# Performance work log

Hardware: AMD Instinct MI355X
Metric: run time of the kernel (lower is better)

## Reference

```python
import jax, jax.numpy as jnp
import numpy as np

DIM = 1024
BATCH = 16384
NUM_LAYERS = 6
S_E = 0.1   # strength_entail
S_C = 0.1   # strength_contra
S_N = 0.05  # strength_neutral
S_NB = 0.05 # strength_neutral_boost
EPS = 1e-12


def _normalize(x, axis=-1):
    # matches F.normalize: x / max(||x||, eps)
    n = jnp.sqrt(jnp.sum(x * x, axis=axis, keepdims=True))
    return x / jnp.maximum(n, EPS)


def setup_inputs() -> dict:
    key = jax.random.key(0)
    ks = jax.random.split(key, 8)
    return {
        "h0": jax.random.normal(ks[0], (BATCH, DIM), dtype=jnp.float32),
        "W1": jax.random.normal(ks[1], (DIM, DIM), dtype=jnp.float32) * 0.02,
        "b1": jnp.zeros((DIM,), dtype=jnp.float32),
        "W2": jax.random.normal(ks[2], (DIM, DIM), dtype=jnp.float32) * 0.02,
        "b2": jnp.zeros((DIM,), dtype=jnp.float32),
        "anchor_entail": jax.random.normal(ks[3], (DIM,), dtype=jnp.float32),
        "anchor_contra": jax.random.normal(ks[4], (DIM,), dtype=jnp.float32),
        "anchor_neutral": jax.random.normal(ks[5], (DIM,), dtype=jnp.float32),
    }


def reference(h0, W1, b1, W2, b2, anchor_entail, anchor_contra, anchor_neutral):
    # Static collapse with three fixed anchors (rot_rank=0, adaptive_metric=False).
    e_dir = _normalize(anchor_entail, axis=0)   # [D]
    c_dir = _normalize(anchor_contra, axis=0)
    n_dir = _normalize(anchor_neutral, axis=0)

    h = h0
    for _ in range(NUM_LAYERS):
        h_n = _normalize(h)                      # [B, D]
        a_e = h_n @ e_dir                        # [B]
        a_c = h_n @ c_dir
        a_n = h_n @ n_dir
        # divergence_from_alignment: div = 1 - align
        div_e = 1.0 - a_e
        div_c = 1.0 - a_c
        div_n = 1.0 - a_n

        # small MLP update: Linear -> Tanh -> Linear (torch Linear: x @ W.T + b)
        delta = jnp.tanh(h @ W1.T + b1) @ W2.T + b2

        # per-anchor force directions: normalize(h - anchor_dir)
        f_e = _normalize(h - e_dir)
        f_c = _normalize(h - c_dir)
        f_n = _normalize(h - n_dir)

        # boundary_proximity(a_e, a_c): 1 when equidistant from E and C
        boundary = jnp.clip(1.0 - jnp.abs(a_e - a_c), 0.0, 1.0)  # [B]

        h = (h + delta
             - S_E * div_e[:, None] * f_e
             - S_C * div_c[:, None] * f_c
             - S_N * div_n[:, None] * f_n
             - S_NB * boundary[:, None] * f_n)

        # norm clamp at 10 (soft rescale, as in the torch code)
        h_norm = jnp.sqrt(jnp.sum(h * h, axis=-1, keepdims=True))
        h = jnp.where(h_norm > 10.0, h * (10.0 / (h_norm + 1e-8)), h)
    return h
```

## Files before the change

### kernel.cpp

```cpp
#include <hip/hip_runtime.h>
#include <hip/hip_bf16.h>
#include <math.h>

#define DIM 1024
#define BATCH 16384
#define NLAYER 6

typedef __bf16 bf16_t;
typedef __attribute__((ext_vector_type(8))) __bf16 bf16x8;
typedef __attribute__((ext_vector_type(4))) float f32x4;

__device__ __forceinline__ void gload16(const void* g, void* l) {
  __builtin_amdgcn_global_load_lds(
      (const __attribute__((address_space(1))) void*)g,
      (__attribute__((address_space(3))) void*)l, 16, 0, 0);
}

__device__ __forceinline__ float fast_tanh(float x) {
  x = fminf(9.f, fmaxf(-9.f, x));
  const float e = __expf(x + x);
  return (e - 1.f) * __builtin_amdgcn_rcpf(e + 1.f);
}

__device__ __forceinline__ float bf2f(unsigned short u) {
  return __uint_as_float(((unsigned int)u) << 16);
}

template <int MODE>
__global__ __launch_bounds__(256, 4) void gemm_kernel(
    const bf16_t* __restrict__ A, const bf16_t* __restrict__ W,
    const float* __restrict__ bias, bf16_t* __restrict__ outB,
    float* __restrict__ outF, const f32x4* __restrict__ coef,
    const f32x4* __restrict__ colpack, const float* __restrict__ scaleArr,
    const bf16_t* __restrict__ hbIn) {
  __shared__ __align__(16) bf16_t sA[128 * 64];
  __shared__ __align__(16) bf16_t sB[128 * 64];
  const int tid = threadIdx.x;
  const int w = tid >> 6;
  const int lane = tid & 63;
  const int bm = blockIdx.x * 128;
  const int bn = blockIdx.y * 128;
  const int wm = (w & 1) * 64;
  const int wn = (w >> 1) * 64;
  const int lm = lane & 15;
  const int lc = lane >> 4;

  f32x4 acc[4][4] = {};

  const int srow = tid >> 3;
  const int swz = ((tid & 7) ^ (srow & 7)) * 8;
  const bf16_t* gA = A + (size_t)(bm + srow) * DIM + swz;
  const bf16_t* gW = W + (size_t)(bn + srow) * DIM + swz;
  char* lA = (char*)sA + w * 1024;
  char* lB = (char*)sB + w * 1024;

  for (int kt = 0; kt < DIM; kt += 64) {
#pragma unroll
    for (int q = 0; q < 4; ++q) {
      gload16(gA + kt + (size_t)q * 32 * DIM, lA + q * 4096);
      gload16(gW + kt + (size_t)q * 32 * DIM, lB + q * 4096);
    }
    __syncthreads();
#pragma unroll
    for (int kh = 0; kh < 2; ++kh) {
      bf16x8 aF[4], bF[4];
      const int lgc = kh * 4 + lc;
#pragma unroll
      for (int i = 0; i < 4; ++i) {
        const int rowA = wm + i * 16 + lm;
        aF[i] = *(const bf16x8*)((char*)sA + rowA * 128 +
                                 ((lgc ^ (lm & 7)) << 4));
      }
#pragma unroll
      for (int j = 0; j < 4; ++j) {
        const int rowB = wn + j * 16 + lm;
        bF[j] = *(const bf16x8*)((char*)sB + rowB * 128 +
                                 ((lgc ^ (lm & 7)) << 4));
      }
#pragma unroll
      for (int i = 0; i < 4; ++i)
#pragma unroll
        for (int j = 0; j < 4; ++j)
          acc[i][j] = __builtin_amdgcn_mfma_f32_16x16x32_bf16(
              aF[i], bF[j], acc[i][j], 0, 0, 0);
    }
    __syncthreads();
  }

  const int r0 = lc << 2;
#pragma unroll
  for (int i = 0; i < 4; ++i) {
    const int rowBase = bm + wm + i * 16 + r0;
    if constexpr (MODE == 0) {
      float s4[4];
#pragma unroll
      for (int r = 0; r < 4; ++r) s4[r] = scaleArr[rowBase + r];
#pragma unroll
      for (int j = 0; j < 4; ++j) {
        const int col = bn + wn + j * 16 + lm;
        const float bv = bias[col];
#pragma unroll
        for (int r = 0; r < 4; ++r)
          outB[(size_t)(rowBase + r) * DIM + col] =
              (bf16_t)fast_tanh(s4[r] * acc[i][j][r] + bv);
      }
    } else {
      f32x4 cf[4];
#pragma unroll
      for (int r = 0; r < 4; ++r) cf[r] = coef[rowBase + r];
#pragma unroll
      for (int j = 0; j < 4; ++j) {
        const int col = bn + wn + j * 16 + lm;
        const f32x4 cp = colpack[col];
#pragma unroll
        for (int r = 0; r < 4; ++r) {
          const size_t idx = (size_t)(rowBase + r) * DIM + col;
          const float hp = (float)hbIn[idx];
          const float v = acc[i][j][r] + cp.w + cf[r].x * cp.x +
                          cf[r].y * cp.y + cf[r].z * cp.z + cf[r].w * hp;
          outB[idx] = (bf16_t)v;
          if constexpr (MODE == 2) outF[idx] = v;
        }
      }
    }
  }
}

template <int IN_FP32>
__global__ __launch_bounds__(256) void stats_kernel(
    const void* __restrict__ src, bf16_t* __restrict__ dstb,
    float* __restrict__ scaleArr, f32x4* __restrict__ coef,
    const float* __restrict__ dirs, int doClamp) {
  const int row = blockIdx.x;
  const int t = threadIdx.x;
  float4 v;
  if constexpr (IN_FP32) {
    v = ((const float4*)src)[(size_t)row * 256 + t];
  } else {
    const ushort4 u = ((const ushort4*)src)[(size_t)row * 256 + t];
    v.x = bf2f(u.x); v.y = bf2f(u.y); v.z = bf2f(u.z); v.w = bf2f(u.w);
  }
  const float4 e = ((const float4*)dirs)[t];
  const float4 c = ((const float4*)dirs)[t + 256];
  const float4 n = ((const float4*)dirs)[t + 512];
  float ss = v.x * v.x + v.y * v.y + v.z * v.z + v.w * v.w;
  float de = v.x * e.x + v.y * e.y + v.z * e.z + v.w * e.w;
  float dc = v.x * c.x + v.y * c.y + v.z * c.z + v.w * c.w;
  float dn = v.x * n.x + v.y * n.y + v.z * n.z + v.w * n.w;
#pragma unroll
  for (int off = 32; off; off >>= 1) {
    ss += __shfl_down(ss, off);
    de += __shfl_down(de, off);
    dc += __shfl_down(dc, off);
    dn += __shfl_down(dn, off);
  }
  __shared__ float red[4][4];
  const int w = t >> 6;
  if ((t & 63) == 0) {
    red[w][0] = ss; red[w][1] = de; red[w][2] = dc; red[w][3] = dn;
  }
  __syncthreads();
  if constexpr (IN_FP32) {
    union { bf16_t b[4]; uint2 u; } pk;
    pk.b[0] = (bf16_t)v.x; pk.b[1] = (bf16_t)v.y;
    pk.b[2] = (bf16_t)v.z; pk.b[3] = (bf16_t)v.w;
    ((uint2*)dstb)[(size_t)row * 256 + t] = pk.u;
  }
  if (t == 0) {
    float S = 0, E = 0, C = 0, N = 0;
#pragma unroll
    for (int i = 0; i < 4; ++i) {
      S += red[i][0]; E += red[i][1]; C += red[i][2]; N += red[i][3];
    }
    const float norm = sqrtf(S);
    float scale = 1.f;
    if (doClamp && norm > 10.f) scale = 10.f / (norm + 1e-8f);
    const float invn = 1.f / fmaxf(norm, 1e-12f);
    const float ae = E * invn;
    const float ac = C * invn;
    const float an = N * invn;
    const float nc = norm * scale;
    const float re = sqrtf(fmaxf(nc * nc - 2.f * nc * ae + 1.f, 0.f));
    const float rc = sqrtf(fmaxf(nc * nc - 2.f * nc * ac + 1.f, 0.f));
    const float rn = sqrtf(fmaxf(nc * nc - 2.f * nc * an + 1.f, 0.f));
    const float boundary = fminf(fmaxf(1.f - fabsf(ae - ac), 0.f), 1.f);
    f32x4 cf;
    cf.x = 0.1f * (1.f - ae) / fmaxf(re, 1e-12f);
    cf.y = 0.1f * (1.f - ac) / fmaxf(rc, 1e-12f);
    cf.z = (0.05f * (1.f - an) + 0.05f * boundary) / fmaxf(rn, 1e-12f);
    cf.w = scale * (1.f - cf.x - cf.y - cf.z);
    coef[row] = cf;
    scaleArr[row] = scale;
  }
}

__global__ __launch_bounds__(256) void finalize_kernel(
    float* __restrict__ outF, const float* __restrict__ scaleArr) {
  const int row = blockIdx.x;
  const int t = threadIdx.x;
  const float s = scaleArr[row];
  float4 v = ((float4*)outF)[(size_t)row * 256 + t];
  v.x *= s; v.y *= s; v.z *= s; v.w *= s;
  ((float4*)outF)[(size_t)row * 256 + t] = v;
}

__global__ __launch_bounds__(256) void prep_dirs(
    const float* __restrict__ ae, const float* __restrict__ ac,
    const float* __restrict__ an, float* __restrict__ dirs) {
  const int t = threadIdx.x;
  const float4 a = ((const float4*)ae)[t];
  const float4 b = ((const float4*)ac)[t];
  const float4 c = ((const float4*)an)[t];
  float sa = a.x * a.x + a.y * a.y + a.z * a.z + a.w * a.w;
  float sb = b.x * b.x + b.y * b.y + b.z * b.z + b.w * b.w;
  float sc = c.x * c.x + c.y * c.y + c.z * c.z + c.w * c.w;
#pragma unroll
  for (int off = 32; off; off >>= 1) {
    sa += __shfl_down(sa, off);
    sb += __shfl_down(sb, off);
    sc += __shfl_down(sc, off);
  }
  __shared__ float red[4][3];
  __shared__ float fin[3];
  const int w = t >> 6;
  if ((t & 63) == 0) { red[w][0] = sa; red[w][1] = sb; red[w][2] = sc; }
  __syncthreads();
  if (t == 0) {
    float x = 0, y = 0, z = 0;
#pragma unroll
    for (int i = 0; i < 4; ++i) { x += red[i][0]; y += red[i][1]; z += red[i][2]; }
    fin[0] = x; fin[1] = y; fin[2] = z;
  }
  __syncthreads();
  const float ia = 1.f / fmaxf(sqrtf(fin[0]), 1e-12f);
  const float ib = 1.f / fmaxf(sqrtf(fin[1]), 1e-12f);
  const float ic = 1.f / fmaxf(sqrtf(fin[2]), 1e-12f);
  float4 oa, ob, oc;
  oa.x = a.x * ia; oa.y = a.y * ia; oa.z = a.z * ia; oa.w = a.w * ia;
  ob.x = b.x * ib; ob.y = b.y * ib; ob.z = b.z * ib; ob.w = b.w * ib;
  oc.x = c.x * ic; oc.y = c.y * ic; oc.z = c.z * ic; oc.w = c.w * ic;
  ((float4*)dirs)[t] = oa;
  ((float4*)dirs)[t + 256] = ob;
  ((float4*)dirs)[t + 512] = oc;
}

__global__ __launch_bounds__(256) void prep_cols(
    const float* __restrict__ dirs, const float* __restrict__ b2,
    f32x4* __restrict__ colpack) {
  const int t = threadIdx.x;
  const float4 e = ((const float4*)dirs)[t];
  const float4 c = ((const float4*)dirs)[t + 256];
  const float4 n = ((const float4*)dirs)[t + 512];
  const float4 b = ((const float4*)b2)[t];
  f32x4 o;
  o.x = e.x; o.y = c.x; o.z = n.x; o.w = b.x; colpack[4 * t + 0] = o;
  o.x = e.y; o.y = c.y; o.z = n.y; o.w = b.y; colpack[4 * t + 1] = o;
  o.x = e.z; o.y = c.z; o.z = n.z; o.w = b.z; colpack[4 * t + 2] = o;
  o.x = e.w; o.y = c.w; o.z = n.w; o.w = b.w; colpack[4 * t + 3] = o;
}

__global__ __launch_bounds__(256) void cast_w_kernel(
    const float* __restrict__ W, bf16_t* __restrict__ Wb) {
  const int i = blockIdx.x * 256 + threadIdx.x;
  const float4 v = ((const float4*)W)[i];
  union { bf16_t b[4]; uint2 u; } pk;
  pk.b[0] = (bf16_t)v.x; pk.b[1] = (bf16_t)v.y;
  pk.b[2] = (bf16_t)v.z; pk.b[3] = (bf16_t)v.w;
  ((uint2*)Wb)[i] = pk.u;
}

extern "C" void kernel_launch(void* const* d_in, const int* in_sizes, int n_in,
                              void* d_out, int out_size, void* d_ws,
                              size_t ws_size, hipStream_t stream) {
  const float* h0 = (const float*)d_in[0];
  const float* W1 = (const float*)d_in[1];
  const float* b1 = (const float*)d_in[2];
  const float* W2 = (const float*)d_in[3];
  const float* b2 = (const float*)d_in[4];
  const float* ae = (const float*)d_in[5];
  const float* ac = (const float*)d_in[6];
  const float* an = (const float*)d_in[7];
  float* outF = (float*)d_out;

  char* ws = (char*)d_ws;
  bf16_t* hb = (bf16_t*)ws;  ws += (size_t)BATCH * DIM * 2;
  bf16_t* Tb = (bf16_t*)ws;  ws += (size_t)BATCH * DIM * 2;
  bf16_t* W1b = (bf16_t*)ws; ws += (size_t)DIM * DIM * 2;
  bf16_t* W2b = (bf16_t*)ws; ws += (size_t)DIM * DIM * 2;
  float* dirs = (float*)ws;  ws += 3 * DIM * 4;
  f32x4* colpack = (f32x4*)ws; ws += DIM * 16;
  f32x4* coef = (f32x4*)ws;  ws += (size_t)BATCH * 16;
  float* scaleArr = (float*)ws; ws += (size_t)BATCH * 4;

  prep_dirs<<<1, 256, 0, stream>>>(ae, ac, an, dirs);
  prep_cols<<<1, 256, 0, stream>>>(dirs, b2, colpack);
  cast_w_kernel<<<DIM * DIM / 1024, 256, 0, stream>>>(W1, W1b);
  cast_w_kernel<<<DIM * DIM / 1024, 256, 0, stream>>>(W2, W2b);
  stats_kernel<1><<<BATCH, 256, 0, stream>>>(h0, hb, scaleArr, coef, dirs, 0);

  dim3 grid(BATCH / 128, DIM / 128);
  for (int l = 0; l < NLAYER; ++l) {
    gemm_kernel<0><<<grid, 256, 0, stream>>>(hb, W1b, b1, Tb, nullptr, nullptr,
                                             nullptr, scaleArr, nullptr);
    if (l < NLAYER - 1) {
      gemm_kernel<1><<<grid, 256, 0, stream>>>(Tb, W2b, b2, hb, nullptr, coef,
                                               colpack, nullptr, hb);
      stats_kernel<0><<<BATCH, 256, 0, stream>>>(hb, nullptr, scaleArr, coef,
                                                 dirs, 1);
    } else {
      gemm_kernel<2><<<grid, 256, 0, stream>>>(Tb, W2b, b2, hb, outF, coef,
                                               colpack, nullptr, hb);
      stats_kernel<0><<<BATCH, 256, 0, stream>>>(hb, nullptr, scaleArr, coef,
                                                 dirs, 1);
      finalize_kernel<<<BATCH, 256, 0, stream>>>(outF, scaleArr);
    }
  }
}
```

Measured before the change: 748.3 us.

## Use 256x256 double-buffered GEMM tiles with 8 waves and interleaved prefetch

Each GEMM block now computes a 256x256 tile with 512 threads instead of 128x128 with 256 threads. LDS is double-buffered so the next K-slice is fetched with global_load_lds while the current slice feeds the MFMAs, and the loads are split across sub-phases with barriers and setprio. The goal is more operand reuse per byte loaded and less exposed load latency. In exchange it uses 128KB of LDS and more accumulator registers per thread, which lowers occupancy, and the grid shrinks to 256 blocks.

```diff
diff --git a/kernel.cpp b/kernel.cpp
--- a/kernel.cpp
+++ b/kernel.cpp
@@ -27,96 +27,134 @@
 }
 
 template <int MODE>
-__global__ __launch_bounds__(256, 4) void gemm_kernel(
+__global__ __launch_bounds__(512, 2) void gemm_kernel(
     const bf16_t* __restrict__ A, const bf16_t* __restrict__ W,
     const float* __restrict__ bias, bf16_t* __restrict__ outB,
     float* __restrict__ outF, const f32x4* __restrict__ coef,
     const f32x4* __restrict__ colpack, const float* __restrict__ scaleArr,
     const bf16_t* __restrict__ hbIn) {
-  __shared__ __align__(16) bf16_t sA[128 * 64];
-  __shared__ __align__(16) bf16_t sB[128 * 64];
+  __shared__ __align__(16) bf16_t sA[2][256 * 64];
+  __shared__ __align__(16) bf16_t sB[2][256 * 64];
   const int tid = threadIdx.x;
   const int w = tid >> 6;
   const int lane = tid & 63;
-  const int bm = blockIdx.x * 128;
-  const int bn = blockIdx.y * 128;
-  const int wm = (w & 1) * 64;
-  const int wn = (w >> 1) * 64;
+  const int bm = blockIdx.x * 256;
+  const int bn = blockIdx.y * 256;
+  const int wm = (w & 1);
+  const int wn = (w >> 1);
   const int lm = lane & 15;
   const int lc = lane >> 4;
 
-  f32x4 acc[4][4] = {};
+  f32x4 acc[8][4] = {};
 
   const int srow = tid >> 3;
   const int swz = ((tid & 7) ^ (srow & 7)) * 8;
   const bf16_t* gA = A + (size_t)(bm + srow) * DIM + swz;
   const bf16_t* gW = W + (size_t)(bn + srow) * DIM + swz;
-  char* lA = (char*)sA + w * 1024;
-  char* lB = (char*)sB + w * 1024;
-
-  for (int kt = 0; kt < DIM; kt += 64) {
-#pragma unroll
-    for (int q = 0; q < 4; ++q) {
-      gload16(gA + kt + (size_t)q * 32 * DIM, lA + q * 4096);
-      gload16(gW + kt + (size_t)q * 32 * DIM, lB + q * 4096);
+  char* ldA = (char*)&sA[0][0] + w * 1024;
+  char* ldB = (char*)&sB[0][0] + w * 1024;
+
+  const char* rdA = (const char*)&sA[0][0];
+  const char* rdB = (const char*)&sB[0][0];
+  int aRow[8], bRow[4], chOff[2];
+#pragma unroll
+  for (int m = 0; m < 8; ++m) aRow[m] = (wm * 128 + m * 16 + lm) * 128;
+#pragma unroll
+  for (int n = 0; n < 4; ++n) bRow[n] = (wn * 64 + n * 16 + lm) * 128;
+#pragma unroll
+  for (int kh = 0; kh < 2; ++kh)
+    chOff[kh] = ((kh * 4 + lc) ^ (lm & 7)) * 16;
+
+#pragma unroll
+  for (int q = 0; q < 4; ++q) {
+    gload16(gA + (size_t)q * 64 * DIM, ldA + q * 8192);
+    gload16(gW + (size_t)q * 64 * DIM, ldB + q * 8192);
+  }
+  asm volatile("s_waitcnt vmcnt(0)" ::: "memory");
+  __builtin_amdgcn_s_barrier();
+
+  for (int kt = 0; kt < DIM / 64; ++kt) {
+    const int cur = kt & 1;
+    const char* cA = rdA + cur * 32768;
+    const char* cB = rdB + cur * 32768;
+    const bool next = (kt + 1) < (DIM / 64);
+    const int koff = (kt + 1) * 64;
+#pragma unroll
+    for (int p = 0; p < 4; ++p) {
+      const int mh = p >> 1, nh = p & 1;
+      bf16x8 aF[4][2], bF[2][2];
+#pragma unroll
+      for (int m = 0; m < 4; ++m)
+#pragma unroll
+        for (int kh = 0; kh < 2; ++kh)
+          aF[m][kh] = *(const bf16x8*)(cA + aRow[mh * 4 + m] + chOff[kh]);
+#pragma unroll
+      for (int n = 0; n < 2; ++n)
+#pragma unroll
+        for (int kh = 0; kh < 2; ++kh)
+          bF[n][kh] = *(const bf16x8*)(cB + bRow[nh * 2 + n] + chOff[kh]);
+      if (p == 0 && next) {
+        char* d = ldA + (cur ^ 1) * 32768;
+#pragma unroll
+        for (int q = 0; q < 4; ++q)
+          gload16(gA + koff + (size_t)q * 64 * DIM, d + q * 8192);
+      }
+      if (p == 1 && next) {
+        char* d = ldB + (cur ^ 1) * 32768;
+#pragma unroll
+        for (int q = 0; q < 4; ++q)
+          gload16(gW + koff + (size_t)q * 64 * DIM, d + q * 8192);
+      }
+      __builtin_amdgcn_sched_barrier(0);
+      __builtin_amdgcn_s_barrier();
+      asm volatile("s_waitcnt lgkmcnt(0)" ::: "memory");
+      __builtin_amdgcn_sched_barrier(0);
+      __builtin_amdgcn_s_setprio(1);
+#pragma unroll
+      for (int m = 0; m < 4; ++m)
+#pragma unroll
+        for (int n = 0; n < 2; ++n)
+#pragma unroll
+          for (int kh = 0; kh < 2; ++kh)
+            acc[mh * 4 + m][nh * 2 + n] =
+                __builtin_amdgcn_mfma_f32_16x16x32_bf16(
+                    aF[m][kh], bF[n][kh], acc[mh * 4 + m][nh * 2 + n], 0, 0, 0);
+      __builtin_amdgcn_s_setprio(0);
+      if (p == 3) asm volatile("s_waitcnt vmcnt(0)" ::: "memory");
+      __builtin_amdgcn_s_barrier();
     }
-    __syncthreads();
-#pragma unroll
-    for (int kh = 0; kh < 2; ++kh) {
-      bf16x8 aF[4], bF[4];
-      const int lgc = kh * 4 + lc;
-#pragma unroll
-      for (int i = 0; i < 4; ++i) {
-        const int rowA = wm + i * 16 + lm;
-        aF[i] = *(const bf16x8*)((char*)sA + rowA * 128 +
-                                 ((lgc ^ (lm & 7)) << 4));
-      }
-#pragma unroll
-      for (int j = 0; j < 4; ++j) {
-        const int rowB = wn + j * 16 + lm;
-        bF[j] = *(const bf16x8*)((char*)sB + rowB * 128 +
-                                 ((lgc ^ (lm & 7)) << 4));
-      }
-#pragma unroll
-      for (int i = 0; i < 4; ++i)
-#pragma unroll
-        for (int j = 0; j < 4; ++j)
-          acc[i][j] = __builtin_amdgcn_mfma_f32_16x16x32_bf16(
-              aF[i], bF[j], acc[i][j], 0, 0, 0);
-    }
-    __syncthreads();
   }
 
   const int r0 = lc << 2;
 #pragma unroll
-  for (int i = 0; i < 4; ++i) {
-    const int rowBase = bm + wm + i * 16 + r0;
+  for (int m = 0; m < 8; ++m) {
+    const int rowBase = bm + wm * 128 + m * 16 + r0;
     if constexpr (MODE == 0) {
       float s4[4];
 #pragma unroll
       for (int r = 0; r < 4; ++r) s4[r] = scaleArr[rowBase + r];
 #pragma unroll
-      for (int j = 0; j < 4; ++j) {
-        const int col = bn + wn + j * 16 + lm;
+      for (int n = 0; n < 4; ++n) {
+        const int col = bn + wn * 64 + n * 16 + lm;
         const float bv = bias[col];
 #pragma unroll
         for (int r = 0; r < 4; ++r)
           outB[(size_t)(rowBase + r) * DIM + col] =
-              (bf16_t)fast_tanh(s4[r] * acc[i][j][r] + bv);
+              (bf16_t)fast_tanh(s4[r] * acc[m][n][r] + bv);
       }
     } else {
       f32x4 cf[4];
 #pragma unroll
       for (int r = 0; r < 4; ++r) cf[r] = coef[rowBase + r];
 #pragma unroll
-      for (int j = 0; j < 4; ++j) {
-        const int col = bn + wn + j * 16 + lm;
+      for (int n = 0; n < 4; ++n) {
+        const int col = bn + wn * 64 + n * 16 + lm;
         const f32x4 cp = colpack[col];
 #pragma unroll
         for (int r = 0; r < 4; ++r) {
           const size_t idx = (size_t)(rowBase + r) * DIM + col;
           const float hp = (float)hbIn[idx];
-          const float v = acc[i][j][r] + cp.w + cf[r].x * cp.x +
+          const float v = acc[m][n][r] + cp.w + cf[r].x * cp.x +
                           cf[r].y * cp.y + cf[r].z * cp.z + cf[r].w * hp;
           outB[idx] = (bf16_t)v;
           if constexpr (MODE == 2) outF[idx] = v;
@@ -298,17 +336,17 @@
   cast_w_kernel<<<DIM * DIM / 1024, 256, 0, stream>>>(W2, W2b);
   stats_kernel<1><<<BATCH, 256, 0, stream>>>(h0, hb, scaleArr, coef, dirs, 0);
 
-  dim3 grid(BATCH / 128, DIM / 128);
+  dim3 grid(BATCH / 256, DIM / 256);
   for (int l = 0; l < NLAYER; ++l) {
-    gemm_kernel<0><<<grid, 256, 0, stream>>>(hb, W1b, b1, Tb, nullptr, nullptr,
+    gemm_kernel<0><<<grid, 512, 0, stream>>>(hb, W1b, b1, Tb, nullptr, nullptr,
                                              nullptr, scaleArr, nullptr);
     if (l < NLAYER - 1) {
-      gemm_kernel<1><<<grid, 256, 0, stream>>>(Tb, W2b, b2, hb, nullptr, coef,
+      gemm_kernel<1><<<grid, 512, 0, stream>>>(Tb, W2b, b2, hb, nullptr, coef,
                                                colpack, nullptr, hb);
       stats_kernel<0><<<BATCH, 256, 0, stream>>>(hb, nullptr, scaleArr, coef,
                                                  dirs, 1);
     } else {
-      gemm_kernel<2><<<grid, 256, 0, stream>>>(Tb, W2b, b2, hb, outF, coef,
+      gemm_kernel<2><<<grid, 512, 0, stream>>>(Tb, W2b, b2, hb, outF, coef,
                                                colpack, nullptr, hb);
       stats_kernel<0><<<BATCH, 256, 0, stream>>>(hb, nullptr, scaleArr, coef,
                                                  dirs, 1);
```

Measured after the change: 843.9 us. 12.8% more time.

## Fuse row stats into GEMM2 epilogue with atomics and LDS-staged vector stores

Applied to the files above, without the earlier changes.

The per-row norm and anchor-dot reductions move into the second GEMM's epilogue. Each block computes partial sums and accumulates them into a global buffer with atomics, and a small convert kernel turns the sums into coefficients. This removes the separate stats pass that re-read hb every layer. The epilogue also stages the accumulators through LDS so each lane writes 16 contiguous bf16 values, and blocks are remapped by XCD for L2 locality. In exchange it adds atomic traffic and fp32 summation order nondeterminism, and it computes the stats from fp32 values instead of the bf16-rounded h.

```diff
diff --git a/kernel.cpp b/kernel.cpp
--- a/kernel.cpp
+++ b/kernel.cpp
@@ -32,14 +32,20 @@
     const float* __restrict__ bias, bf16_t* __restrict__ outB,
     float* __restrict__ outF, const f32x4* __restrict__ coef,
     const f32x4* __restrict__ colpack, const float* __restrict__ scaleArr,
-    const bf16_t* __restrict__ hbIn) {
-  __shared__ __align__(16) bf16_t sA[128 * 64];
-  __shared__ __align__(16) bf16_t sB[128 * 64];
+    const bf16_t* __restrict__ hbIn, float* __restrict__ sums) {
+  __shared__ __align__(16) char smem[34816];
+  bf16_t* sA = (bf16_t*)smem;
+  bf16_t* sB = (bf16_t*)(smem + 16384);
   const int tid = threadIdx.x;
   const int w = tid >> 6;
   const int lane = tid & 63;
-  const int bm = blockIdx.x * 128;
-  const int bn = blockIdx.y * 128;
+  const int id = blockIdx.x;
+  const int xcd = id & 7;
+  const int jj_ = id >> 3;
+  const int bxi = (xcd << 4) + (jj_ >> 3);
+  const int byi = jj_ & 7;
+  const int bm = bxi * 128;
+  const int bn = byi * 128;
   const int wm = (w & 1) * 64;
   const int wn = (w >> 1) * 64;
   const int lm = lane & 15;
@@ -87,59 +93,131 @@
     __syncthreads();
   }
 
+  float* epi = (float*)(smem + w * 8704);
   const int r0 = lc << 2;
+  const int rr = lane >> 2;
+  const int cc = (lane & 3) << 4;
+  const int gcol = bn + wn + cc;
+
 #pragma unroll
   for (int i = 0; i < 4; ++i) {
-    const int rowBase = bm + wm + i * 16 + r0;
+    float* eb = epi + (i & 1) * 1088;
+#pragma unroll
+    for (int j = 0; j < 4; ++j)
+#pragma unroll
+      for (int r = 0; r < 4; ++r)
+        eb[(r0 + r) * 68 + (j << 4) + lm] = acc[i][j][r];
+    asm volatile("s_waitcnt lgkmcnt(0)" ::: "memory");
+    const float* src = eb + rr * 68 + cc;
+    f32x4 v[4];
+#pragma unroll
+    for (int q = 0; q < 4; ++q) v[q] = *(const f32x4*)(src + 4 * q);
+
+    const int grow = bm + wm + i * 16 + rr;
     if constexpr (MODE == 0) {
-      float s4[4];
-#pragma unroll
-      for (int r = 0; r < 4; ++r) s4[r] = scaleArr[rowBase + r];
-#pragma unroll
-      for (int j = 0; j < 4; ++j) {
-        const int col = bn + wn + j * 16 + lm;
-        const float bv = bias[col];
-#pragma unroll
-        for (int r = 0; r < 4; ++r)
-          outB[(size_t)(rowBase + r) * DIM + col] =
-              (bf16_t)fast_tanh(s4[r] * acc[i][j][r] + bv);
-      }
+      const float s = scaleArr[grow];
+      union { bf16_t b[16]; uint4 u[2]; } pk;
+#pragma unroll
+      for (int q = 0; q < 4; ++q) {
+        const f32x4 bv = *(const f32x4*)(bias + gcol + 4 * q);
+#pragma unroll
+        for (int j = 0; j < 4; ++j)
+          pk.b[4 * q + j] = (bf16_t)fast_tanh(s * v[q][j] + bv[j]);
+      }
+      uint4* dst = (uint4*)(outB + (size_t)grow * DIM + gcol);
+      dst[0] = pk.u[0];
+      dst[1] = pk.u[1];
     } else {
-      f32x4 cf[4];
-#pragma unroll
-      for (int r = 0; r < 4; ++r) cf[r] = coef[rowBase + r];
-#pragma unroll
-      for (int j = 0; j < 4; ++j) {
-        const int col = bn + wn + j * 16 + lm;
-        const f32x4 cp = colpack[col];
-#pragma unroll
-        for (int r = 0; r < 4; ++r) {
-          const size_t idx = (size_t)(rowBase + r) * DIM + col;
-          const float hp = (float)hbIn[idx];
-          const float v = acc[i][j][r] + cp.w + cf[r].x * cp.x +
-                          cf[r].y * cp.y + cf[r].z * cp.z + cf[r].w * hp;
-          outB[idx] = (bf16_t)v;
-          if constexpr (MODE == 2) outF[idx] = v;
+      const f32x4 cf = coef[grow];
+      const bf16_t* hp = hbIn + (size_t)grow * DIM + gcol;
+      union { bf16_t b[16]; uint4 u[2]; } hin;
+      hin.u[0] = *(const uint4*)hp;
+      hin.u[1] = *(const uint4*)(hp + 8);
+      union { bf16_t b[16]; uint4 u[2]; } pk;
+      float ss = 0.f, de = 0.f, dc = 0.f, dn = 0.f;
+      f32x4 fo[4];
+#pragma unroll
+      for (int q = 0; q < 4; ++q)
+#pragma unroll
+        for (int j = 0; j < 4; ++j) {
+          const int e = 4 * q + j;
+          const f32x4 cp = colpack[gcol + e];
+          const float val = v[q][j] + cp.w + cf.x * cp.x + cf.y * cp.y +
+                            cf.z * cp.z + cf.w * (float)hin.b[e];
+          pk.b[e] = (bf16_t)val;
+          fo[q][j] = val;
+          ss += val * val;
+          de += val * cp.x;
+          dc += val * cp.y;
+          dn += val * cp.z;
         }
-      }
-    }
-  }
-}
-
-template <int IN_FP32>
-__global__ __launch_bounds__(256) void stats_kernel(
-    const void* __restrict__ src, bf16_t* __restrict__ dstb,
+      uint4* dst = (uint4*)(outB + (size_t)grow * DIM + gcol);
+      dst[0] = pk.u[0];
+      dst[1] = pk.u[1];
+      if constexpr (MODE == 2) {
+#pragma unroll
+        for (int q = 0; q < 4; ++q)
+          *(f32x4*)(outF + (size_t)grow * DIM + gcol + 4 * q) = fo[q];
+      }
+      ss += __shfl_xor(ss, 1); ss += __shfl_xor(ss, 2);
+      de += __shfl_xor(de, 1); de += __shfl_xor(de, 2);
+      dc += __shfl_xor(dc, 1); dc += __shfl_xor(dc, 2);
+      dn += __shfl_xor(dn, 1); dn += __shfl_xor(dn, 2);
+      if ((lane & 3) == 0) {
+        float* sp = sums + (size_t)grow * 4;
+        atomicAdd(sp + 0, ss);
+        atomicAdd(sp + 1, de);
+        atomicAdd(sp + 2, dc);
+        atomicAdd(sp + 3, dn);
+      }
+    }
+  }
+}
+
+__global__ __launch_bounds__(256) void convert_kernel(
+    float* __restrict__ sums, f32x4* __restrict__ coef,
+    float* __restrict__ scaleArr) {
+  const int row = blockIdx.x * 256 + threadIdx.x;
+  f32x4* sp = (f32x4*)(sums + (size_t)row * 4);
+  const f32x4 s = *sp;
+  f32x4 z = {};
+  *sp = z;
+  const float S = s.x, E = s.y, C = s.z, N = s.w;
+  const float norm = sqrtf(S);
+  float scale = 1.f;
+  if (norm > 10.f) scale = 10.f / (norm + 1e-8f);
+  const float invn = 1.f / fmaxf(norm, 1e-12f);
+  const float ae = E * invn;
+  const float ac = C * invn;
+  const float an = N * invn;
+  const float nc = norm * scale;
+  const float re = sqrtf(fmaxf(nc * nc - 2.f * nc * ae + 1.f, 0.f));
+  const float rc = sqrtf(fmaxf(nc * nc - 2.f * nc * ac + 1.f, 0.f));
+  const float rn = sqrtf(fmaxf(nc * nc - 2.f * nc * an + 1.f, 0.f));
+  const float boundary = fminf(fmaxf(1.f - fabsf(ae - ac), 0.f), 1.f);
+  f32x4 cf;
+  cf.x = 0.1f * (1.f - ae) / fmaxf(re, 1e-12f);
+  cf.y = 0.1f * (1.f - ac) / fmaxf(rc, 1e-12f);
+  cf.z = (0.05f * (1.f - an) + 0.05f * boundary) / fmaxf(rn, 1e-12f);
+  cf.w = scale * (1.f - cf.x - cf.y - cf.z);
+  coef[row] = cf;
+  scaleArr[row] = scale;
+}
+
+__global__ __launch_bounds__(256) void zero_sums_kernel(
+    float* __restrict__ sums) {
+  const int i = blockIdx.x * 256 + threadIdx.x;
+  f32x4 z = {};
+  ((f32x4*)sums)[i] = z;
+}
+
+__global__ __launch_bounds__(256) void stats0_kernel(
+    const float* __restrict__ src, bf16_t* __restrict__ dstb,
     float* __restrict__ scaleArr, f32x4* __restrict__ coef,
-    const float* __restrict__ dirs, int doClamp) {
+    const float* __restrict__ dirs) {
   const int row = blockIdx.x;
   const int t = threadIdx.x;
-  float4 v;
-  if constexpr (IN_FP32) {
-    v = ((const float4*)src)[(size_t)row * 256 + t];
-  } else {
-    const ushort4 u = ((const ushort4*)src)[(size_t)row * 256 + t];
-    v.x = bf2f(u.x); v.y = bf2f(u.y); v.z = bf2f(u.z); v.w = bf2f(u.w);
-  }
+  const float4 v = ((const float4*)src)[(size_t)row * 256 + t];
   const float4 e = ((const float4*)dirs)[t];
   const float4 c = ((const float4*)dirs)[t + 256];
   const float4 n = ((const float4*)dirs)[t + 512];
@@ -160,12 +238,10 @@
     red[w][0] = ss; red[w][1] = de; red[w][2] = dc; red[w][3] = dn;
   }
   __syncthreads();
-  if constexpr (IN_FP32) {
-    union { bf16_t b[4]; uint2 u; } pk;
-    pk.b[0] = (bf16_t)v.x; pk.b[1] = (bf16_t)v.y;
-    pk.b[2] = (bf16_t)v.z; pk.b[3] = (bf16_t)v.w;
-    ((uint2*)dstb)[(size_t)row * 256 + t] = pk.u;
-  }
+  union { bf16_t b[4]; uint2 u; } pk;
+  pk.b[0] = (bf16_t)v.x; pk.b[1] = (bf16_t)v.y;
+  pk.b[2] = (bf16_t)v.z; pk.b[3] = (bf16_t)v.w;
+  ((uint2*)dstb)[(size_t)row * 256 + t] = pk.u;
   if (t == 0) {
     float S = 0, E = 0, C = 0, N = 0;
 #pragma unroll
@@ -173,8 +249,7 @@
       S += red[i][0]; E += red[i][1]; C += red[i][2]; N += red[i][3];
     }
     const float norm = sqrtf(S);
-    float scale = 1.f;
-    if (doClamp && norm > 10.f) scale = 10.f / (norm + 1e-8f);
+    const float scale = 1.f;
     const float invn = 1.f / fmaxf(norm, 1e-12f);
     const float ae = E * invn;
     const float ac = C * invn;
@@ -291,27 +366,28 @@
   f32x4* colpack = (f32x4*)ws; ws += DIM * 16;
   f32x4* coef = (f32x4*)ws;  ws += (size_t)BATCH * 16;
   float* scaleArr = (float*)ws; ws += (size_t)BATCH * 4;
+  float* sums = (float*)ws;  ws += (size_t)BATCH * 16;
 
   prep_dirs<<<1, 256, 0, stream>>>(ae, ac, an, dirs);
   prep_cols<<<1, 256, 0, stream>>>(dirs, b2, colpack);
   cast_w_kernel<<<DIM * DIM / 1024, 256, 0, stream>>>(W1, W1b);
   cast_w_kernel<<<DIM * DIM / 1024, 256, 0, stream>>>(W2, W2b);
-  stats_kernel<1><<<BATCH, 256, 0, stream>>>(h0, hb, scaleArr, coef, dirs, 0);
-
-  dim3 grid(BATCH / 128, DIM / 128);
+  zero_sums_kernel<<<BATCH / 256, 256, 0, stream>>>(sums);
+  stats0_kernel<<<BATCH, 256, 0, stream>>>(h0, hb, scaleArr, coef, dirs);
+
+  const int grid = (BATCH / 128) * (DIM / 128);
   for (int l = 0; l < NLAYER; ++l) {
     gemm_kernel<0><<<grid, 256, 0, stream>>>(hb, W1b, b1, Tb, nullptr, nullptr,
-                                             nullptr, scaleArr, nullptr);
+                                             nullptr, scaleArr, nullptr,
+                                             nullptr);
     if (l < NLAYER - 1) {
       gemm_kernel<1><<<grid, 256, 0, stream>>>(Tb, W2b, b2, hb, nullptr, coef,
-                                               colpack, nullptr, hb);
-      stats_kernel<0><<<BATCH, 256, 0, stream>>>(hb, nullptr, scaleArr, coef,
-                                                 dirs, 1);
+                                               colpack, nullptr, hb, sums);
+      convert_kernel<<<BATCH / 256, 256, 0, stream>>>(sums, coef, scaleArr);
     } else {
       gemm_kernel<2><<<grid, 256, 0, stream>>>(Tb, W2b, b2, hb, outF, coef,
-                                               colpack, nullptr, hb);
-      stats_kernel<0><<<BATCH, 256, 0, stream>>>(hb, nullptr, scaleArr, coef,
-                                                 dirs, 1);
+                                               colpack, nullptr, hb, sums);
+      convert_kernel<<<BATCH / 256, 256, 0, stream>>>(sums, coef, scaleArr);
       finalize_kernel<<<BATCH, 256, 0, stream>>>(outF, scaleArr);
     }
   }
```

After: 964.5 us. +28.9%, slower.

## Fuse per-row norm and anchor dot reductions into GEMM2 epilogue

Applied to the files above, without the earlier changes.

The second GEMM's epilogue now accumulates per-row sum of squares and dot products with the three anchor directions. It reduces them across the 16 lanes and writes partials per column block into a workspace. A small convert kernel sums the 16 partials per row and computes the clamp scale and force coefficients. This replaces the full stats pass that re-read hb in bf16 after every layer, and the last layer no longer writes hb. Stats are now computed from fp32 values before bf16 rounding, and the epilogue gains extra registers and shuffles.

```diff
diff --git a/kernel.cpp b/kernel.cpp
--- a/kernel.cpp
+++ b/kernel.cpp
@@ -32,7 +32,7 @@
     const float* __restrict__ bias, bf16_t* __restrict__ outB,
     float* __restrict__ outF, const f32x4* __restrict__ coef,
     const f32x4* __restrict__ colpack, const float* __restrict__ scaleArr,
-    const bf16_t* __restrict__ hbIn) {
+    const bf16_t* __restrict__ hbIn, float* __restrict__ part) {
   __shared__ __align__(16) bf16_t sA[128 * 64];
   __shared__ __align__(16) bf16_t sB[128 * 64];
   const int tid = threadIdx.x;
@@ -40,6 +40,7 @@
   const int lane = tid & 63;
   const int bm = blockIdx.x * 128;
   const int bn = blockIdx.y * 128;
+  const int byi = blockIdx.y;
   const int wm = (w & 1) * 64;
   const int wn = (w >> 1) * 64;
   const int lm = lane & 15;
@@ -108,6 +109,7 @@
       f32x4 cf[4];
 #pragma unroll
       for (int r = 0; r < 4; ++r) cf[r] = coef[rowBase + r];
+      float ss[4] = {}, de[4] = {}, dc[4] = {}, dn[4] = {};
 #pragma unroll
       for (int j = 0; j < 4; ++j) {
         const int col = bn + wn + j * 16 + lm;
@@ -118,28 +120,74 @@
           const float hp = (float)hbIn[idx];
           const float v = acc[i][j][r] + cp.w + cf[r].x * cp.x +
                           cf[r].y * cp.y + cf[r].z * cp.z + cf[r].w * hp;
-          outB[idx] = (bf16_t)v;
+          if constexpr (MODE == 1) outB[idx] = (bf16_t)v;
           if constexpr (MODE == 2) outF[idx] = v;
+          ss[r] += v * v;
+          de[r] += v * cp.x;
+          dc[r] += v * cp.y;
+          dn[r] += v * cp.z;
         }
       }
-    }
-  }
-}
-
-template <int IN_FP32>
-__global__ __launch_bounds__(256) void stats_kernel(
-    const void* __restrict__ src, bf16_t* __restrict__ dstb,
+      const int slot = byi * 2 + (w >> 1);
+#pragma unroll
+      for (int r = 0; r < 4; ++r) {
+        float a = ss[r], b = de[r], c = dc[r], d = dn[r];
+#pragma unroll
+        for (int mask = 1; mask < 16; mask <<= 1) {
+          a += __shfl_xor(a, mask);
+          b += __shfl_xor(b, mask);
+          c += __shfl_xor(c, mask);
+          d += __shfl_xor(d, mask);
+        }
+        if (lm == 0) {
+          f32x4 o;
+          o.x = a; o.y = b; o.z = c; o.w = d;
+          ((f32x4*)part)[(size_t)(rowBase + r) * 16 + slot] = o;
+        }
+      }
+    }
+  }
+}
+
+__global__ __launch_bounds__(256) void convert_kernel(
+    const float* __restrict__ part, f32x4* __restrict__ coef,
+    float* __restrict__ scaleArr) {
+  const int row = blockIdx.x * 256 + threadIdx.x;
+  const f32x4* p = (const f32x4*)part + (size_t)row * 16;
+  float S = 0.f, E = 0.f, C = 0.f, N = 0.f;
+#pragma unroll
+  for (int b = 0; b < 16; ++b) {
+    const f32x4 v = p[b];
+    S += v.x; E += v.y; C += v.z; N += v.w;
+  }
+  const float norm = sqrtf(S);
+  float scale = 1.f;
+  if (norm > 10.f) scale = 10.f / (norm + 1e-8f);
+  const float invn = 1.f / fmaxf(norm, 1e-12f);
+  const float ae = E * invn;
+  const float ac = C * invn;
+  const float an = N * invn;
+  const float nc = norm * scale;
+  const float re = sqrtf(fmaxf(nc * nc - 2.f * nc * ae + 1.f, 0.f));
+  const float rc = sqrtf(fmaxf(nc * nc - 2.f * nc * ac + 1.f, 0.f));
+  const float rn = sqrtf(fmaxf(nc * nc - 2.f * nc * an + 1.f, 0.f));
+  const float boundary = fminf(fmaxf(1.f - fabsf(ae - ac), 0.f), 1.f);
+  f32x4 cf;
+  cf.x = 0.1f * (1.f - ae) / fmaxf(re, 1e-12f);
+  cf.y = 0.1f * (1.f - ac) / fmaxf(rc, 1e-12f);
+  cf.z = (0.05f * (1.f - an) + 0.05f * boundary) / fmaxf(rn, 1e-12f);
+  cf.w = scale * (1.f - cf.x - cf.y - cf.z);
+  coef[row] = cf;
+  scaleArr[row] = scale;
+}
+
+__global__ __launch_bounds__(256) void stats0_kernel(
+    const float* __restrict__ src, bf16_t* __restrict__ dstb,
     float* __restrict__ scaleArr, f32x4* __restrict__ coef,
-    const float* __restrict__ dirs, int doClamp) {
+    const float* __restrict__ dirs) {
   const int row = blockIdx.x;
   const int t = threadIdx.x;
-  float4 v;
-  if constexpr (IN_FP32) {
-    v = ((const float4*)src)[(size_t)row * 256 + t];
-  } else {
-    const ushort4 u = ((const ushort4*)src)[(size_t)row * 256 + t];
-    v.x = bf2f(u.x); v.y = bf2f(u.y); v.z = bf2f(u.z); v.w = bf2f(u.w);
-  }
+  const float4 v = ((const float4*)src)[(size_t)row * 256 + t];
   const float4 e = ((const float4*)dirs)[t];
   const float4 c = ((const float4*)dirs)[t + 256];
   const float4 n = ((const float4*)dirs)[t + 512];
@@ -160,12 +208,10 @@
     red[w][0] = ss; red[w][1] = de; red[w][2] = dc; red[w][3] = dn;
   }
   __syncthreads();
-  if constexpr (IN_FP32) {
-    union { bf16_t b[4]; uint2 u; } pk;
-    pk.b[0] = (bf16_t)v.x; pk.b[1] = (bf16_t)v.y;
-    pk.b[2] = (bf16_t)v.z; pk.b[3] = (bf16_t)v.w;
-    ((uint2*)dstb)[(size_t)row * 256 + t] = pk.u;
-  }
+  union { bf16_t b[4]; uint2 u; } pk;
+  pk.b[0] = (bf16_t)v.x; pk.b[1] = (bf16_t)v.y;
+  pk.b[2] = (bf16_t)v.z; pk.b[3] = (bf16_t)v.w;
+  ((uint2*)dstb)[(size_t)row * 256 + t] = pk.u;
   if (t == 0) {
     float S = 0, E = 0, C = 0, N = 0;
 #pragma unroll
@@ -173,8 +219,7 @@
       S += red[i][0]; E += red[i][1]; C += red[i][2]; N += red[i][3];
     }
     const float norm = sqrtf(S);
-    float scale = 1.f;
-    if (doClamp && norm > 10.f) scale = 10.f / (norm + 1e-8f);
+    const float scale = 1.f;
     const float invn = 1.f / fmaxf(norm, 1e-12f);
     const float ae = E * invn;
     const float ac = C * invn;
@@ -291,27 +336,27 @@
   f32x4* colpack = (f32x4*)ws; ws += DIM * 16;
   f32x4* coef = (f32x4*)ws;  ws += (size_t)BATCH * 16;
   float* scaleArr = (float*)ws; ws += (size_t)BATCH * 4;
+  float* part = (float*)ws;  ws += (size_t)BATCH * 16 * 16;
 
   prep_dirs<<<1, 256, 0, stream>>>(ae, ac, an, dirs);
   prep_cols<<<1, 256, 0, stream>>>(dirs, b2, colpack);
   cast_w_kernel<<<DIM * DIM / 1024, 256, 0, stream>>>(W1, W1b);
   cast_w_kernel<<<DIM * DIM / 1024, 256, 0, stream>>>(W2, W2b);
-  stats_kernel<1><<<BATCH, 256, 0, stream>>>(h0, hb, scaleArr, coef, dirs, 0);
+  stats0_kernel<<<BATCH, 256, 0, stream>>>(h0, hb, scaleArr, coef, dirs);
 
   dim3 grid(BATCH / 128, DIM / 128);
   for (int l = 0; l < NLAYER; ++l) {
     gemm_kernel<0><<<grid, 256, 0, stream>>>(hb, W1b, b1, Tb, nullptr, nullptr,
-                                             nullptr, scaleArr, nullptr);
+                                             nullptr, scaleArr, nullptr,
+                                             nullptr);
     if (l < NLAYER - 1) {
       gemm_kernel<1><<<grid, 256, 0, stream>>>(Tb, W2b, b2, hb, nullptr, coef,
-                                               colpack, nullptr, hb);
-      stats_kernel<0><<<BATCH, 256, 0, stream>>>(hb, nullptr, scaleArr, coef,
-                                                 dirs, 1);
+                                               colpack, nullptr, hb, part);
+      convert_kernel<<<BATCH / 256, 256, 0, stream>>>(part, coef, scaleArr);
     } else {
-      gemm_kernel<2><<<grid, 256, 0, stream>>>(Tb, W2b, b2, hb, outF, coef,
-                                               colpack, nullptr, hb);
-      stats_kernel<0><<<BATCH, 256, 0, stream>>>(hb, nullptr, scaleArr, coef,
-                                                 dirs, 1);
+      gemm_kernel<2><<<grid, 256, 0, stream>>>(Tb, W2b, b2, nullptr, outF, coef,
+                                               colpack, nullptr, hb, part);
+      convert_kernel<<<BATCH / 256, 256, 0, stream>>>(part, coef, scaleArr);
       finalize_kernel<<<BATCH, 256, 0, stream>>>(outF, scaleArr);
     }
   }
```

After: 763.6 us. 1.02x slower.
